# Optimization experiments

Hardware: AMD Instinct MI355X
Metric: run time of the kernel (lower is better)

The kernel has to match this reference:

```python
import jax, jax.numpy as jnp
import numpy as np

D_MODEL = 768
N_HEAD = 12
HEAD_DIM = D_MODEL // N_HEAD
SCALE = HEAD_DIM ** -0.5
B, T = 8, 1024
NEG_INF = -1e9


def setup_inputs() -> dict:
    key = jax.random.key(0)
    ks = jax.random.split(key, 4)
    x = jax.random.normal(ks[0], (B, T, D_MODEL), dtype=jnp.float32)
    W_attn = jax.random.normal(ks[1], (D_MODEL, 3 * D_MODEL), dtype=jnp.float32) * 0.02
    b_attn = jnp.zeros((3 * D_MODEL,), dtype=jnp.float32)
    W_proj = jax.random.normal(ks[2], (D_MODEL, D_MODEL), dtype=jnp.float32) * 0.02
    b_proj = jnp.zeros((D_MODEL,), dtype=jnp.float32)
    return {"x": x, "W_attn": W_attn, "b_attn": b_attn, "W_proj": W_proj, "b_proj": b_proj}


def reference(x, W_attn, b_attn, W_proj, b_proj):
    Bn, Tn, C = x.shape
    # fused QKV projection: [B,T,3C]
    qkv = jnp.einsum('btc,cd->btd', x, W_attn) + b_attn
    q, k, v = jnp.split(qkv, 3, axis=-1)
    # [B, H, T, hd]
    def heads(t):
        return t.reshape(Bn, Tn, N_HEAD, HEAD_DIM).transpose(0, 2, 1, 3)
    q, k, v = heads(q), heads(k), heads(v)
    # scaled dot-product scores [B,H,T,T]
    att = jnp.einsum('bhqd,bhkd->bhqk', q, k) * SCALE
    # causal mask: mask[i,j]=1 where j>i (upper triangle, excluded)
    causal = jnp.tril(jnp.ones((Tn, Tn), dtype=bool))
    att = jnp.where(causal[None, None, :, :], att, NEG_INF)
    att = jax.nn.softmax(att, axis=-1)
    # weighted value sum -> merge heads
    y = jnp.einsum('bhqk,bhkd->bhqd', att, v)
    y = y.transpose(0, 2, 1, 3).reshape(Bn, Tn, C)
    # output projection
    return jnp.einsum('btc,cd->btd', y, W_proj) + b_proj
```

## Files before the change

### kernel.cpp

```cpp
#include <hip/hip_runtime.h>
#include <hip/hip_bf16.h>

#define T_SEQ 1024
#define NBATCH 8
#define NHEAD 12
#define HD 64
#define CDIM 768
#define C3 2304

typedef __attribute__((ext_vector_type(8))) __bf16 bf16x8;
typedef __attribute__((ext_vector_type(4))) __bf16 bf16x4;
typedef __attribute__((ext_vector_type(2))) __bf16 bf16x2;
typedef __attribute__((ext_vector_type(4))) float  f32x4;
typedef __attribute__((ext_vector_type(16))) float f32x16;

__device__ __forceinline__ f32x4 mfma_bf16(bf16x8 a, bf16x8 b, f32x4 c) {
    return __builtin_amdgcn_mfma_f32_16x16x32_bf16(a, b, c, 0, 0, 0);
}
__device__ __forceinline__ f32x16 mfma32(bf16x8 a, bf16x8 b, f32x16 c) {
    return __builtin_amdgcn_mfma_f32_32x32x16_bf16(a, b, c, 0, 0, 0);
}

__device__ __forceinline__ void gload16(const void* g, void* l) {
    __builtin_amdgcn_global_load_lds(
        (const __attribute__((address_space(1))) unsigned int*)g,
        (__attribute__((address_space(3))) unsigned int*)l, 16, 0, 0);
}

#define WAIT_VM(N)  asm volatile("s_waitcnt vmcnt(" #N ")" ::: "memory")
#define WAIT_LGKM0  asm volatile("s_waitcnt lgkmcnt(0)" ::: "memory")

__global__ __launch_bounds__(256) void cvt_f32_bf16(const float* __restrict__ in,
                                                    __bf16* __restrict__ out, int n4) {
    int i = blockIdx.x * 256 + threadIdx.x;
    if (i < n4) {
        float4 v = ((const float4*)in)[i];
        bf16x4 o = { (__bf16)v.x, (__bf16)v.y, (__bf16)v.z, (__bf16)v.w };
        ((bf16x4*)out)[i] = o;
    }
}

__global__ __launch_bounds__(256) void transpose_cvt2(const float* __restrict__ Wa,
                                                      __bf16* __restrict__ Wat,
                                                      const float* __restrict__ Wp,
                                                      __bf16* __restrict__ Wpt) {
    __shared__ float tile[32][33];
    const int bx = blockIdx.x;
    const float* W;  __bf16* Wt;  int C, c0;
    if (bx < 72) { W = Wa; Wt = Wat; C = 2304; c0 = bx * 32; }
    else         { W = Wp; Wt = Wpt; C = 768;  c0 = (bx - 72) * 32; }
    const int r0 = blockIdx.y * 32;
    const int tc = threadIdx.x & 31, tr = threadIdx.x >> 5;
#pragma unroll
    for (int i = 0; i < 4; ++i)
        tile[tr + i * 8][tc] = W[(size_t)(r0 + tr + i * 8) * C + c0 + tc];
    __syncthreads();
#pragma unroll
    for (int i = 0; i < 4; ++i)
        Wt[(size_t)(c0 + tr + i * 8) * 768 + r0 + tc] = (__bf16)tile[tc][tr + i * 8];
}

template<int OUT_BF16>
__global__ __launch_bounds__(256) void gemm_bt(const __bf16* __restrict__ A,
                                               const __bf16* __restrict__ Bt,
                                               const float* __restrict__ bias,
                                               void* __restrict__ Cout,
                                               int M, int N, int K, int nbx) {
    __shared__ __align__(16) __bf16 sA[3][128 * 32];
    __shared__ __align__(16) __bf16 sB[3][128 * 32];
    const int t = threadIdx.x, l = t & 63, w = t >> 6;
    const int l31 = l & 31, lh = l >> 5;
    const int wr = w >> 1, wc = w & 1;
    const int xcd = blockIdx.x & 7;
    const int local = blockIdx.x >> 3;
    const int m0 = (xcd * 8 + (local & 7)) * 128;
    const int n0 = (local >> 3) * 128;

    const int r_st = t >> 2;
    const int sw_st = (r_st & 3) ^ ((r_st >> 2) & 3);
    const int g_off = ((t & 3) ^ sw_st) << 3;
    const int sw_rd = (l31 & 3) ^ ((l31 >> 2) & 3);

    f32x16 acc[2][2];
#pragma unroll
    for (int m = 0; m < 2; ++m)
#pragma unroll
        for (int n = 0; n < 2; ++n)
#pragma unroll
            for (int r = 0; r < 16; ++r) acc[m][n][r] = 0.f;

    const int nk = K >> 5;

#pragma unroll
    for (int s = 0; s < 3; ++s) {
        const int k0 = s << 5;
#pragma unroll
        for (int i = 0; i < 2; ++i) {
            int r = i * 64 + r_st;
            gload16(A + (size_t)(m0 + r) * K + k0 + g_off,
                    (char*)&sA[s][0] + (i * 256 + w * 64) * 16);
            gload16(Bt + (size_t)(n0 + r) * K + k0 + g_off,
                    (char*)&sB[s][0] + (i * 256 + w * 64) * 16);
        }
    }

    int cur = 0;
    for (int kt = 0; kt < nk; ++kt) {
        if (kt + 2 < nk)      WAIT_VM(8);
        else if (kt + 1 < nk) WAIT_VM(4);
        else                  WAIT_VM(0);
        __builtin_amdgcn_s_barrier();

        bf16x8 af[2][2], bg[2][2];
#pragma unroll
        for (int m = 0; m < 2; ++m)
#pragma unroll
            for (int ks = 0; ks < 2; ++ks)
                af[m][ks] = *(const bf16x8*)(&sA[cur][(wr * 64 + m * 32 + l31) * 32
                                                      + ((((ks << 1) | lh) ^ sw_rd) << 3)]);
#pragma unroll
        for (int n = 0; n < 2; ++n)
#pragma unroll
            for (int ks = 0; ks < 2; ++ks)
                bg[n][ks] = *(const bf16x8*)(&sB[cur][(wc * 64 + n * 32 + l31) * 32
                                                      + ((((ks << 1) | lh) ^ sw_rd) << 3)]);

#pragma unroll
        for (int ks = 0; ks < 2; ++ks)
#pragma unroll
            for (int m = 0; m < 2; ++m)
#pragma unroll
                for (int n = 0; n < 2; ++n)
                    acc[m][n] = mfma32(af[m][ks], bg[n][ks], acc[m][n]);

        WAIT_LGKM0;
        __builtin_amdgcn_s_barrier();

        if (kt + 3 < nk) {
            const int k0 = (kt + 3) << 5;
#pragma unroll
            for (int i = 0; i < 2; ++i) {
                int r = i * 64 + r_st;
                gload16(A + (size_t)(m0 + r) * K + k0 + g_off,
                        (char*)&sA[cur][0] + (i * 256 + w * 64) * 16);
                gload16(Bt + (size_t)(n0 + r) * K + k0 + g_off,
                        (char*)&sB[cur][0] + (i * 256 + w * 64) * 16);
            }
        }
        cur = (cur == 2) ? 0 : cur + 1;
    }

#pragma unroll
    for (int n = 0; n < 2; ++n) {
        int col = n0 + wc * 64 + n * 32 + l31;
        float bv = bias[col];
#pragma unroll
        for (int m = 0; m < 2; ++m) {
            int rbase = m0 + wr * 64 + m * 32 + 4 * lh;
#pragma unroll
            for (int r = 0; r < 16; ++r) {
                int row = rbase + (r & 3) + 8 * (r >> 2);
                float v = acc[m][n][r] + bv;
                if (OUT_BF16)
                    ((__bf16*)Cout)[(size_t)row * N + col] = (__bf16)v;
                else
                    ((float*)Cout)[(size_t)row * N + col] = v;
            }
        }
    }
}

__global__ __launch_bounds__(256, 2) void attn_fwd(const __bf16* __restrict__ qkv,
                                                   __bf16* __restrict__ y) {
    const int tid = threadIdx.x, l = tid & 63, w = tid >> 6;
    const int lr = l & 15, lk = l >> 4;
    const int r7 = lr & 7;
    const int bid = blockIdx.x;
    const int pr = bid / 96;
    const int hb = bid % 96;
    const int h = hb % NHEAD;
    const int b = hb / NHEAD;

    __shared__ __align__(16) __bf16 sK[2][64][64];
    __shared__ __align__(16) __bf16 sV[2][64][64];
    __shared__ __align__(16) __bf16 sP[4][16][72];

    const size_t baseQ = (size_t)b * T_SEQ * C3 + h * HD;
    const __bf16* Kp = qkv + baseQ + CDIM;
    const __bf16* Vp = qkv + baseQ + 2 * CDIM;

    const int vk0 = tid >> 3;
    const int vc = (tid & 7) << 3;
    const int vg = tid & 7;
    const int krow = tid >> 3;
    const int kchunk = (tid & 7) ^ ((tid >> 3) & 7);

#pragma unroll 1
    for (int job = 0; job < 2; ++job) {
        const int qt = (job == 0) ? pr : 15 - pr;
        const int q0 = qt * 64;
        const int nt = qt + 1;
        const int q_abs = q0 + w * 16 + lr;

        const size_t rowQ = baseQ + (size_t)(q0 + w * 16 + lr) * C3;
        bf16x8 qa0 = *(const bf16x8*)(qkv + rowQ + lk * 8);
        bf16x8 qa1 = *(const bf16x8*)(qkv + rowQ + 32 + lk * 8);
#pragma unroll
        for (int e = 0; e < 8; ++e) {
            qa0[e] = (__bf16)((float)qa0[e] * 0.125f);
            qa1[e] = (__bf16)((float)qa1[e] * 0.125f);
        }

        f32x4 acc[4];
#pragma unroll
        for (int fd = 0; fd < 4; ++fd) acc[fd] = f32x4{0.f, 0.f, 0.f, 0.f};
        float mrun = -1e30f, lrun = 0.f;

        bf16x8 vreg[2];
#pragma unroll
        for (int i = 0; i < 2; ++i)
            vreg[i] = *(const bf16x8*)(Vp + (size_t)(i * 32 + vk0) * C3 + vc);
#pragma unroll
        for (int i = 0; i < 2; ++i)
            gload16(Kp + (size_t)(i * 32 + krow) * C3 + kchunk * 8,
                    (char*)&sK[0][0][0] + (i * 256 + w * 64) * 16);
#pragma unroll
        for (int i = 0; i < 2; ++i) {
            int key = i * 32 + vk0;
#pragma unroll
            for (int e = 0; e < 8; ++e)
                sV[0][vc + e][key ^ ((e ^ vg) << 3)] = vreg[i][e];
        }
        __syncthreads();

#pragma unroll 1
        for (int t = 0; t < nt; ++t) {
            const int kv0 = t * 64;
            const int cur = t & 1, nxt = cur ^ 1;
            const bool pre = (t + 1 < nt);
            if (pre) {
                const int kvp = kv0 + 64;
#pragma unroll
                for (int i = 0; i < 2; ++i)
                    vreg[i] = *(const bf16x8*)(Vp + (size_t)(kvp + i * 32 + vk0) * C3 + vc);
#pragma unroll
                for (int i = 0; i < 2; ++i)
                    gload16(Kp + (size_t)(kvp + i * 32 + krow) * C3 + kchunk * 8,
                            (char*)&sK[nxt][0][0] + (i * 256 + w * 64) * 16);
            }
            f32x4 s[4];
            __builtin_amdgcn_s_setprio(1);
#pragma unroll
            for (int fc = 0; fc < 4; ++fc) {
                const __bf16* kr = &sK[cur][fc * 16 + lr][0];
                bf16x8 k0 = *(const bf16x8*)(kr + ((lk ^ r7) << 3));
                bf16x8 k1 = *(const bf16x8*)(kr + (((4 + lk) ^ r7) << 3));
                f32x4 z = f32x4{0.f, 0.f, 0.f, 0.f};
                z = mfma_bf16(k0, qa0, z);
                z = mfma_bf16(k1, qa1, z);
                s[fc] = z;
            }
            __builtin_amdgcn_s_setprio(0);
            float ps[4][4];
#pragma unroll
            for (int fc = 0; fc < 4; ++fc)
#pragma unroll
                for (int j = 0; j < 4; ++j) ps[fc][j] = s[fc][j];
            if (t == nt - 1) {
#pragma unroll
                for (int fc = 0; fc < 4; ++fc)
#pragma unroll
                    for (int j = 0; j < 4; ++j) {
                        int key = kv0 + fc * 16 + lk * 4 + j;
                        if (key > q_abs) ps[fc][j] = -1e30f;
                    }
            }
            float mfc[4];
#pragma unroll
            for (int fc = 0; fc < 4; ++fc)
                mfc[fc] = fmaxf(fmaxf(ps[fc][0], ps[fc][1]), fmaxf(ps[fc][2], ps[fc][3]));
            float mt = fmaxf(fmaxf(mfc[0], mfc[1]), fmaxf(mfc[2], mfc[3]));
            mt = fmaxf(mt, __shfl_xor(mt, 16, 64));
            mt = fmaxf(mt, __shfl_xor(mt, 32, 64));
            if (!__all(mt - mrun <= 8.f)) {
                const float mn = fmaxf(mrun, mt);
                const float corr = __expf(mrun - mn);
                mrun = mn;
                lrun *= corr;
                float cj[4];
#pragma unroll
                for (int j = 0; j < 4; ++j) cj[j] = __shfl(corr, lk * 4 + j, 64);
#pragma unroll
                for (int fd = 0; fd < 4; ++fd)
#pragma unroll
                    for (int j = 0; j < 4; ++j) acc[fd][j] *= cj[j];
            }
            float rs = 0.f;
#pragma unroll
            for (int fc = 0; fc < 4; ++fc)
#pragma unroll
                for (int j = 0; j < 4; ++j) {
                    float p = __expf(ps[fc][j] - mrun);
                    ps[fc][j] = p;
                    rs += p;
                }
            rs += __shfl_xor(rs, 16, 64);
            rs += __shfl_xor(rs, 32, 64);
            lrun += rs;
#pragma unroll
            for (int fc = 0; fc < 4; ++fc)
#pragma unroll
                for (int jp = 0; jp < 2; ++jp) {
                    bf16x2 pk = { (__bf16)ps[fc][jp * 2], (__bf16)ps[fc][jp * 2 + 1] };
                    *(bf16x2*)&sP[w][lr][fc * 16 + lk * 4 + jp * 2] = pk;
                }
            __builtin_amdgcn_s_setprio(1);
#pragma unroll
            for (int ks = 0; ks < 2; ++ks) {
                bf16x8 pa = *(const bf16x8*)&sP[w][lr][ks * 32 + lk * 8];
#pragma unroll
                for (int fd = 0; fd < 4; ++fd) {
                    int d = fd * 16 + lr;
                    int sw = ((d & 7) ^ ((d >> 3) & 7)) << 3;
                    bf16x8 vb = *(const bf16x8*)&sV[cur][d][(ks * 32 + lk * 8) ^ sw];
                    acc[fd] = mfma_bf16(pa, vb, acc[fd]);
                }
            }
            __builtin_amdgcn_s_setprio(0);
            if (pre) {
#pragma unroll
                for (int i = 0; i < 2; ++i) {
                    int key = i * 32 + vk0;
#pragma unroll
                    for (int e = 0; e < 8; ++e)
                        sV[nxt][vc + e][key ^ ((e ^ vg) << 3)] = vreg[i][e];
                }
            }
            __syncthreads();
        }

        float linv[4];
#pragma unroll
        for (int j = 0; j < 4; ++j) linv[j] = 1.f / __shfl(lrun, lk * 4 + j, 64);
        const size_t yrow0 = (size_t)(b * T_SEQ + q0 + w * 16 + lk * 4);
#pragma unroll
        for (int fd = 0; fd < 4; ++fd) {
            int col = h * HD + fd * 16 + lr;
#pragma unroll
            for (int j = 0; j < 4; ++j)
                y[(yrow0 + j) * CDIM + col] = (__bf16)(acc[fd][j] * linv[j]);
        }
    }
}

extern "C" void kernel_launch(void* const* d_in, const int* in_sizes, int n_in,
                              void* d_out, int out_size, void* d_ws, size_t ws_size,
                              hipStream_t stream) {
    const float* x      = (const float*)d_in[0];
    const float* W_attn = (const float*)d_in[1];
    const float* b_attn = (const float*)d_in[2];
    const float* W_proj = (const float*)d_in[3];
    const float* b_proj = (const float*)d_in[4];

    __bf16* xb  = (__bf16*)d_ws;
    __bf16* Wat = xb  + (size_t)8192 * 768;
    __bf16* Wpt = Wat + (size_t)2304 * 768;
    __bf16* qkv = Wpt + (size_t)768 * 768;
    __bf16* yb  = qkv + (size_t)8192 * 2304;

    cvt_f32_bf16<<<6144, 256, 0, stream>>>(x, xb, (8192 * 768) / 4);
    transpose_cvt2<<<dim3(96, 24), 256, 0, stream>>>(W_attn, Wat, W_proj, Wpt);

    gemm_bt<1><<<18 * 64, 256, 0, stream>>>(xb, Wat, b_attn, (void*)qkv, 8192, 2304, 768, 18);
    attn_fwd<<<NBATCH * NHEAD * 8, 256, 0, stream>>>(qkv, yb);
    gemm_bt<0><<<6 * 64, 256, 0, stream>>>(yb, Wpt, b_proj, d_out, 8192, 768, 768, 6);
}
```

Baseline: 111.7 us.

## Load QKV GEMM A operand directly to registers, staging only B in LDS

Adds a QKV projection GEMM variant that reads A-operand fragments from global memory straight into registers, double-buffered one k-step ahead, while only the weight tile is staged through LDS with a triple-buffered async pipeline. The aim is to cut LDS traffic and LDS footprint for A and free LDS bandwidth for B reads. In exchange, A reads become uncoalesced-ish per-lane 16B global loads with latency that must be hidden by the one-step prefetch, and the bias-add epilogue uses strided scalar bf16 stores.

```diff
diff --git a/kernel.cpp b/kernel.cpp
--- a/kernel.cpp
+++ b/kernel.cpp
@@ -58,6 +58,111 @@
 #pragma unroll
     for (int i = 0; i < 4; ++i)
         Wt[(size_t)(c0 + tr + i * 8) * 768 + r0 + tc] = (__bf16)tile[tc][tr + i * 8];
+}
+
+#define QKV_STEP(T, AFC, AFN)                                                    \
+    do {                                                                         \
+        const int t_ = (T);                                                      \
+        if (t_ == 0)           WAIT_VM(4);                                       \
+        else if (t_ + 2 < nk)  WAIT_VM(2);                                       \
+        else                   WAIT_VM(0);                                       \
+        __builtin_amdgcn_s_barrier();                                            \
+        if (t_ + 1 < nk) {                                                       \
+            AFN[0][0] = *(const bf16x8*)(pA0 + (t_ + 1) * 32);                   \
+            AFN[0][1] = *(const bf16x8*)(pA0 + (t_ + 1) * 32 + 16);              \
+            AFN[1][0] = *(const bf16x8*)(pA1 + (t_ + 1) * 32);                   \
+            AFN[1][1] = *(const bf16x8*)(pA1 + (t_ + 1) * 32 + 16);              \
+        }                                                                        \
+        bf16x8 bg00 = *(const bf16x8*)(&sB[curb][(wc * 64 + l31) * 32 + ((lh ^ sw_rd) << 3)]);          \
+        bf16x8 bg01 = *(const bf16x8*)(&sB[curb][(wc * 64 + l31) * 32 + (((2 | lh) ^ sw_rd) << 3)]);    \
+        bf16x8 bg10 = *(const bf16x8*)(&sB[curb][(wc * 64 + 32 + l31) * 32 + ((lh ^ sw_rd) << 3)]);     \
+        bf16x8 bg11 = *(const bf16x8*)(&sB[curb][(wc * 64 + 32 + l31) * 32 + (((2 | lh) ^ sw_rd) << 3)]); \
+        acc[0][0] = mfma32(AFC[0][0], bg00, acc[0][0]);                          \
+        acc[0][1] = mfma32(AFC[0][0], bg10, acc[0][1]);                          \
+        acc[1][0] = mfma32(AFC[1][0], bg00, acc[1][0]);                          \
+        acc[1][1] = mfma32(AFC[1][0], bg10, acc[1][1]);                          \
+        acc[0][0] = mfma32(AFC[0][1], bg01, acc[0][0]);                          \
+        acc[0][1] = mfma32(AFC[0][1], bg11, acc[0][1]);                          \
+        acc[1][0] = mfma32(AFC[1][1], bg01, acc[1][0]);                          \
+        acc[1][1] = mfma32(AFC[1][1], bg11, acc[1][1]);                          \
+        WAIT_LGKM0;                                                              \
+        __builtin_amdgcn_s_barrier();                                            \
+        if (t_ + 3 < nk) {                                                       \
+            const int k0 = (t_ + 3) << 5;                                        \
+            gload16(Bt + (size_t)(n0 + r_st) * K + k0 + g_off,                   \
+                    (char*)&sB[curb][0] + (w * 64) * 16);                        \
+            gload16(Bt + (size_t)(n0 + 64 + r_st) * K + k0 + g_off,              \
+                    (char*)&sB[curb][0] + (256 + w * 64) * 16);                  \
+        }                                                                        \
+        curb = (curb == 2) ? 0 : curb + 1;                                       \
+    } while (0)
+
+__global__ __launch_bounds__(256) void gemm_qkv_a2(const __bf16* __restrict__ A,
+                                                   const __bf16* __restrict__ Bt,
+                                                   const float* __restrict__ bias,
+                                                   __bf16* __restrict__ Cout,
+                                                   int M, int N, int K) {
+    __shared__ __align__(16) __bf16 sB[3][128 * 32];
+    const int t = threadIdx.x, l = t & 63, w = t >> 6;
+    const int l31 = l & 31, lh = l >> 5;
+    const int wr = w >> 1, wc = w & 1;
+    const int xcd = blockIdx.x & 7;
+    const int local = blockIdx.x >> 3;
+    const int m0 = (xcd * 8 + (local & 7)) * 128;
+    const int n0 = (local >> 3) * 128;
+
+    const int r_st = t >> 2;
+    const int sw_st = (r_st & 3) ^ ((r_st >> 2) & 3);
+    const int g_off = ((t & 3) ^ sw_st) << 3;
+    const int sw_rd = (l31 & 3) ^ ((l31 >> 2) & 3);
+
+    const __bf16* pA0 = A + (size_t)(m0 + wr * 64 + l31) * K + lh * 8;
+    const __bf16* pA1 = pA0 + (size_t)32 * K;
+
+    f32x16 acc[2][2];
+#pragma unroll
+    for (int m = 0; m < 2; ++m)
+#pragma unroll
+        for (int n = 0; n < 2; ++n)
+#pragma unroll
+            for (int r = 0; r < 16; ++r) acc[m][n][r] = 0.f;
+
+    const int nk = K >> 5;
+    bf16x8 afA[2][2], afB[2][2];
+
+    afA[0][0] = *(const bf16x8*)(pA0);
+    afA[0][1] = *(const bf16x8*)(pA0 + 16);
+    afA[1][0] = *(const bf16x8*)(pA1);
+    afA[1][1] = *(const bf16x8*)(pA1 + 16);
+#pragma unroll
+    for (int s = 0; s < 3; ++s) {
+        const int k0 = s << 5;
+        gload16(Bt + (size_t)(n0 + r_st) * K + k0 + g_off,
+                (char*)&sB[s][0] + (w * 64) * 16);
+        gload16(Bt + (size_t)(n0 + 64 + r_st) * K + k0 + g_off,
+                (char*)&sB[s][0] + (256 + w * 64) * 16);
+    }
+
+    int curb = 0;
+    for (int kt = 0; kt < nk; kt += 2) {
+        QKV_STEP(kt, afA, afB);
+        QKV_STEP(kt + 1, afB, afA);
+    }
+
+#pragma unroll
+    for (int n = 0; n < 2; ++n) {
+        int col = n0 + wc * 64 + n * 32 + l31;
+        float bv = bias[col];
+#pragma unroll
+        for (int m = 0; m < 2; ++m) {
+            int rbase = m0 + wr * 64 + m * 32 + 4 * lh;
+#pragma unroll
+            for (int r = 0; r < 16; ++r) {
+                int row = rbase + (r & 3) + 8 * (r >> 2);
+                Cout[(size_t)row * N + col] = (__bf16)(acc[m][n][r] + bv);
+            }
+        }
+    }
 }
 
 template<int OUT_BF16>
@@ -371,7 +476,7 @@
     cvt_f32_bf16<<<6144, 256, 0, stream>>>(x, xb, (8192 * 768) / 4);
     transpose_cvt2<<<dim3(96, 24), 256, 0, stream>>>(W_attn, Wat, W_proj, Wpt);
 
-    gemm_bt<1><<<18 * 64, 256, 0, stream>>>(xb, Wat, b_attn, (void*)qkv, 8192, 2304, 768, 18);
+    gemm_qkv_a2<<<18 * 64, 256, 0, stream>>>(xb, Wat, b_attn, qkv, 8192, 2304, 768);
     attn_fwd<<<NBATCH * NHEAD * 8, 256, 0, stream>>>(qkv, yb);
     gemm_bt<0><<<6 * 64, 256, 0, stream>>>(yb, Wpt, b_proj, d_out, 8192, 768, 768, 6);
 }
```

Measured after the change: 139.1 us. +24.5%, slower.

## Add quadrant-staged QKV GEMM kernel with interleaved loads and MFMA

Applied to the files above, without the earlier changes.

Replaces the QKV projection GEMM with a new kernel that uses BK=64 double-buffered LDS tiles split into 64-row halves and XOR-swizzled. The next tile's global-to-LDS loads are issued quadrant by quadrant between MFMA groups, which is meant to overlap memory traffic with compute. It also uses 16x16x32 MFMAs and launch bounds targeting two blocks per CU. The cost is more barriers per k-step and a more intricate wait-count schedule that has to stay correct.

```diff
diff --git a/kernel.cpp b/kernel.cpp
--- a/kernel.cpp
+++ b/kernel.cpp
@@ -58,6 +58,124 @@
 #pragma unroll
     for (int i = 0; i < 4; ++i)
         Wt[(size_t)(c0 + tr + i * 8) * 768 + r0 + tc] = (__bf16)tile[tc][tr + i * 8];
+}
+
+__global__ __launch_bounds__(256, 2) void gemm_qkv4(const __bf16* __restrict__ A,
+                                                    const __bf16* __restrict__ Bt,
+                                                    const float* __restrict__ bias,
+                                                    __bf16* __restrict__ Cout,
+                                                    int M, int N, int K) {
+    __shared__ __align__(16) __bf16 sA[2][2][64 * 64];
+    __shared__ __align__(16) __bf16 sB[2][2][64 * 64];
+    const int t = threadIdx.x, l = t & 63, w = t >> 6;
+    const int lr = l & 15, lk = l >> 4;
+    const int r7 = lr & 7;
+    const int wr = w >> 1, wc = w & 1;
+    const int xcd = blockIdx.x & 7;
+    const int local = blockIdx.x >> 3;
+    const int m0 = (xcd * 8 + (local & 7)) * 128;
+    const int n0 = (local >> 3) * 128;
+
+    const int srow = t >> 3;
+    const int g_off = (((t & 7) ^ (srow & 7)) << 3);
+
+#define STG_A(slot, half, kt)                                                      \
+    { _Pragma("unroll") for (int i_ = 0; i_ < 2; ++i_)                             \
+        gload16(A + (size_t)(m0 + (half) * 64 + i_ * 32 + srow) * K + ((kt) << 6) + g_off, \
+                (char*)&sA[slot][half][0] + (i_ * 256 + w * 64) * 16); }
+#define STG_B(slot, half, kt)                                                      \
+    { _Pragma("unroll") for (int i_ = 0; i_ < 2; ++i_)                             \
+        gload16(Bt + (size_t)(n0 + (half) * 64 + i_ * 32 + srow) * K + ((kt) << 6) + g_off, \
+                (char*)&sB[slot][half][0] + (i_ * 256 + w * 64) * 16); }
+#define RD_A(slot, mf, ks) (*(const bf16x8*)&sA[slot][(mf) >> 1]                   \
+        [(wr * 32 + ((mf) & 1) * 16 + lr) * 64 + (((((ks) << 2) | lk) ^ r7) << 3)])
+#define RD_B(slot, nf, ks) (*(const bf16x8*)&sB[slot][(nf) >> 1]                   \
+        [(wc * 32 + ((nf) & 1) * 16 + lr) * 64 + (((((ks) << 2) | lk) ^ r7) << 3)])
+
+    f32x4 acc[4][4];
+#pragma unroll
+    for (int m = 0; m < 4; ++m)
+#pragma unroll
+        for (int n = 0; n < 4; ++n) acc[m][n] = f32x4{0.f, 0.f, 0.f, 0.f};
+
+    const int nk = K >> 6;
+
+    STG_A(0, 0, 0); STG_B(0, 0, 0); STG_B(0, 1, 0); STG_A(0, 1, 0);
+
+    bf16x8 af[4][2], bg[4][2];
+#pragma unroll 1
+    for (int kt = 0; kt < nk; ++kt) {
+        const int sl = kt & 1, ns = sl ^ 1;
+        const bool st = (kt + 1 < nk);
+        WAIT_VM(4);
+        __builtin_amdgcn_s_barrier();
+#pragma unroll
+        for (int ks = 0; ks < 2; ++ks) {
+            af[0][ks] = RD_A(sl, 0, ks);  af[1][ks] = RD_A(sl, 1, ks);
+            bg[0][ks] = RD_B(sl, 0, ks);  bg[1][ks] = RD_B(sl, 1, ks);
+        }
+        if (st) STG_A(ns, 0, kt + 1);
+#pragma unroll
+        for (int ks = 0; ks < 2; ++ks)
+#pragma unroll
+            for (int mf = 0; mf < 2; ++mf)
+#pragma unroll
+                for (int nf = 0; nf < 2; ++nf)
+                    acc[mf][nf] = mfma_bf16(af[mf][ks], bg[nf][ks], acc[mf][nf]);
+        if (st) { WAIT_VM(4); } else { WAIT_VM(2); }
+        __builtin_amdgcn_s_barrier();
+#pragma unroll
+        for (int ks = 0; ks < 2; ++ks) {
+            bg[2][ks] = RD_B(sl, 2, ks);  bg[3][ks] = RD_B(sl, 3, ks);
+        }
+        if (st) STG_B(ns, 0, kt + 1);
+#pragma unroll
+        for (int ks = 0; ks < 2; ++ks)
+#pragma unroll
+            for (int mf = 0; mf < 2; ++mf)
+#pragma unroll
+                for (int nf = 2; nf < 4; ++nf)
+                    acc[mf][nf] = mfma_bf16(af[mf][ks], bg[nf][ks], acc[mf][nf]);
+        if (st) { WAIT_VM(4); } else { WAIT_VM(0); }
+        __builtin_amdgcn_s_barrier();
+#pragma unroll
+        for (int ks = 0; ks < 2; ++ks) {
+            af[2][ks] = RD_A(sl, 2, ks);  af[3][ks] = RD_A(sl, 3, ks);
+        }
+        if (st) STG_B(ns, 1, kt + 1);
+#pragma unroll
+        for (int ks = 0; ks < 2; ++ks)
+#pragma unroll
+            for (int mf = 2; mf < 4; ++mf)
+#pragma unroll
+                for (int nf = 0; nf < 2; ++nf)
+                    acc[mf][nf] = mfma_bf16(af[mf][ks], bg[nf][ks], acc[mf][nf]);
+        if (st) STG_A(ns, 1, kt + 1);
+#pragma unroll
+        for (int ks = 0; ks < 2; ++ks)
+#pragma unroll
+            for (int mf = 2; mf < 4; ++mf)
+#pragma unroll
+                for (int nf = 2; nf < 4; ++nf)
+                    acc[mf][nf] = mfma_bf16(af[mf][ks], bg[nf][ks], acc[mf][nf]);
+    }
+
+#pragma unroll
+    for (int nf = 0; nf < 4; ++nf) {
+        int col = n0 + (nf >> 1) * 64 + wc * 32 + (nf & 1) * 16 + lr;
+        float bv = bias[col];
+#pragma unroll
+        for (int mf = 0; mf < 4; ++mf) {
+            int row0 = m0 + (mf >> 1) * 64 + wr * 32 + (mf & 1) * 16 + lk * 4;
+#pragma unroll
+            for (int j = 0; j < 4; ++j)
+                Cout[(size_t)(row0 + j) * N + col] = (__bf16)(acc[mf][nf][j] + bv);
+        }
+    }
+#undef STG_A
+#undef STG_B
+#undef RD_A
+#undef RD_B
 }
 
 template<int OUT_BF16>
@@ -371,7 +489,7 @@
     cvt_f32_bf16<<<6144, 256, 0, stream>>>(x, xb, (8192 * 768) / 4);
     transpose_cvt2<<<dim3(96, 24), 256, 0, stream>>>(W_attn, Wat, W_proj, Wpt);
 
-    gemm_bt<1><<<18 * 64, 256, 0, stream>>>(xb, Wat, b_attn, (void*)qkv, 8192, 2304, 768, 18);
+    gemm_qkv4<<<18 * 64, 256, 0, stream>>>(xb, Wat, b_attn, qkv, 8192, 2304, 768);
     attn_fwd<<<NBATCH * NHEAD * 8, 256, 0, stream>>>(qkv, yb);
     gemm_bt<0><<<6 * 64, 256, 0, stream>>>(yb, Wpt, b_proj, d_out, 8192, 768, 768, 6);
 }
```

Result: slower. 115.3 us (+3.2%).

## Merge prep kernels into one launch and shrink GEMM M-tile to 64

Applied to the files above, without the earlier changes.

Combines the x conversion and the weight transpose/convert into a single prep launch, saving one kernel launch. Both GEMMs now use 64x128 tiles instead of 128x128, with an adjusted XCD-aware block mapping and matching vmcnt wait counts. The output-projection GEMM goes from 384 to 768 blocks and the QKV GEMM from 1152 to 2304, which should fill the GPU's compute units better. The cost is less data reuse per tile and more global and LDS traffic per FLOP.

```diff
diff --git a/kernel.cpp b/kernel.cpp
--- a/kernel.cpp
+++ b/kernel.cpp
@@ -30,26 +30,27 @@
 #define WAIT_VM(N)  asm volatile("s_waitcnt vmcnt(" #N ")" ::: "memory")
 #define WAIT_LGKM0  asm volatile("s_waitcnt lgkmcnt(0)" ::: "memory")
 
-__global__ __launch_bounds__(256) void cvt_f32_bf16(const float* __restrict__ in,
-                                                    __bf16* __restrict__ out, int n4) {
-    int i = blockIdx.x * 256 + threadIdx.x;
-    if (i < n4) {
-        float4 v = ((const float4*)in)[i];
-        bf16x4 o = { (__bf16)v.x, (__bf16)v.y, (__bf16)v.z, (__bf16)v.w };
-        ((bf16x4*)out)[i] = o;
-    }
-}
-
-__global__ __launch_bounds__(256) void transpose_cvt2(const float* __restrict__ Wa,
-                                                      __bf16* __restrict__ Wat,
-                                                      const float* __restrict__ Wp,
-                                                      __bf16* __restrict__ Wpt) {
+__global__ __launch_bounds__(256) void prep(const float* __restrict__ x,
+                                            __bf16* __restrict__ xb,
+                                            const float* __restrict__ Wa,
+                                            __bf16* __restrict__ Wat,
+                                            const float* __restrict__ Wp,
+                                            __bf16* __restrict__ Wpt) {
     __shared__ float tile[32][33];
     const int bx = blockIdx.x;
+    if (bx < 6144) {
+        int i = bx * 256 + threadIdx.x;
+        float4 v = ((const float4*)x)[i];
+        bf16x4 o = { (__bf16)v.x, (__bf16)v.y, (__bf16)v.z, (__bf16)v.w };
+        ((bf16x4*)xb)[i] = o;
+        return;
+    }
+    const int b2 = bx - 6144;
+    const int gx = b2 % 96, gy = b2 / 96;
     const float* W;  __bf16* Wt;  int C, c0;
-    if (bx < 72) { W = Wa; Wt = Wat; C = 2304; c0 = bx * 32; }
-    else         { W = Wp; Wt = Wpt; C = 768;  c0 = (bx - 72) * 32; }
-    const int r0 = blockIdx.y * 32;
+    if (gx < 72) { W = Wa; Wt = Wat; C = 2304; c0 = gx * 32; }
+    else         { W = Wp; Wt = Wpt; C = 768;  c0 = (gx - 72) * 32; }
+    const int r0 = gy * 32;
     const int tc = threadIdx.x & 31, tr = threadIdx.x >> 5;
 #pragma unroll
     for (int i = 0; i < 4; ++i)
@@ -61,63 +62,57 @@
 }
 
 template<int OUT_BF16>
-__global__ __launch_bounds__(256) void gemm_bt(const __bf16* __restrict__ A,
+__global__ __launch_bounds__(256) void gemm_64(const __bf16* __restrict__ A,
                                                const __bf16* __restrict__ Bt,
                                                const float* __restrict__ bias,
                                                void* __restrict__ Cout,
-                                               int M, int N, int K, int nbx) {
-    __shared__ __align__(16) __bf16 sA[3][128 * 32];
+                                               int M, int N, int K) {
+    __shared__ __align__(16) __bf16 sA[3][64 * 32];
     __shared__ __align__(16) __bf16 sB[3][128 * 32];
     const int t = threadIdx.x, l = t & 63, w = t >> 6;
     const int l31 = l & 31, lh = l >> 5;
     const int wr = w >> 1, wc = w & 1;
     const int xcd = blockIdx.x & 7;
     const int local = blockIdx.x >> 3;
-    const int m0 = (xcd * 8 + (local & 7)) * 128;
-    const int n0 = (local >> 3) * 128;
+    const int m0 = (xcd * 16 + (local & 15)) * 64;
+    const int n0 = (local >> 4) * 128;
 
     const int r_st = t >> 2;
     const int sw_st = (r_st & 3) ^ ((r_st >> 2) & 3);
     const int g_off = ((t & 3) ^ sw_st) << 3;
     const int sw_rd = (l31 & 3) ^ ((l31 >> 2) & 3);
 
-    f32x16 acc[2][2];
-#pragma unroll
-    for (int m = 0; m < 2; ++m)
-#pragma unroll
-        for (int n = 0; n < 2; ++n)
-#pragma unroll
-            for (int r = 0; r < 16; ++r) acc[m][n][r] = 0.f;
+    f32x16 acc[2];
+#pragma unroll
+    for (int n = 0; n < 2; ++n)
+#pragma unroll
+        for (int r = 0; r < 16; ++r) acc[n][r] = 0.f;
 
     const int nk = K >> 5;
 
 #pragma unroll
     for (int s = 0; s < 3; ++s) {
         const int k0 = s << 5;
-#pragma unroll
-        for (int i = 0; i < 2; ++i) {
-            int r = i * 64 + r_st;
-            gload16(A + (size_t)(m0 + r) * K + k0 + g_off,
-                    (char*)&sA[s][0] + (i * 256 + w * 64) * 16);
-            gload16(Bt + (size_t)(n0 + r) * K + k0 + g_off,
+        gload16(A + (size_t)(m0 + r_st) * K + k0 + g_off,
+                (char*)&sA[s][0] + (w * 64) * 16);
+#pragma unroll
+        for (int i = 0; i < 2; ++i)
+            gload16(Bt + (size_t)(n0 + i * 64 + r_st) * K + k0 + g_off,
                     (char*)&sB[s][0] + (i * 256 + w * 64) * 16);
-        }
     }
 
     int cur = 0;
     for (int kt = 0; kt < nk; ++kt) {
-        if (kt + 2 < nk)      WAIT_VM(8);
-        else if (kt + 1 < nk) WAIT_VM(4);
+        if (kt + 2 < nk)      WAIT_VM(6);
+        else if (kt + 1 < nk) WAIT_VM(3);
         else                  WAIT_VM(0);
         __builtin_amdgcn_s_barrier();
 
-        bf16x8 af[2][2], bg[2][2];
-#pragma unroll
-        for (int m = 0; m < 2; ++m)
-#pragma unroll
-            for (int ks = 0; ks < 2; ++ks)
-                af[m][ks] = *(const bf16x8*)(&sA[cur][(wr * 64 + m * 32 + l31) * 32
-                                                      + ((((ks << 1) | lh) ^ sw_rd) << 3)]);
+        bf16x8 af[2], bg[2][2];
+#pragma unroll
+        for (int ks = 0; ks < 2; ++ks)
+            af[ks] = *(const bf16x8*)(&sA[cur][(wr * 32 + l31) * 32
+                                              + ((((ks << 1) | lh) ^ sw_rd) << 3)]);
 #pragma unroll
         for (int n = 0; n < 2; ++n)
 #pragma unroll
@@ -128,24 +123,20 @@
 #pragma unroll
         for (int ks = 0; ks < 2; ++ks)
 #pragma unroll
-            for (int m = 0; m < 2; ++m)
-#pragma unroll
-                for (int n = 0; n < 2; ++n)
-                    acc[m][n] = mfma32(af[m][ks], bg[n][ks], acc[m][n]);
+            for (int n = 0; n < 2; ++n)
+                acc[n] = mfma32(af[ks], bg[n][ks], acc[n]);
 
         WAIT_LGKM0;
         __builtin_amdgcn_s_barrier();
 
         if (kt + 3 < nk) {
             const int k0 = (kt + 3) << 5;
-#pragma unroll
-            for (int i = 0; i < 2; ++i) {
-                int r = i * 64 + r_st;
-                gload16(A + (size_t)(m0 + r) * K + k0 + g_off,
-                        (char*)&sA[cur][0] + (i * 256 + w * 64) * 16);
-                gload16(Bt + (size_t)(n0 + r) * K + k0 + g_off,
+            gload16(A + (size_t)(m0 + r_st) * K + k0 + g_off,
+                    (char*)&sA[cur][0] + (w * 64) * 16);
+#pragma unroll
+            for (int i = 0; i < 2; ++i)
+                gload16(Bt + (size_t)(n0 + i * 64 + r_st) * K + k0 + g_off,
                         (char*)&sB[cur][0] + (i * 256 + w * 64) * 16);
-            }
         }
         cur = (cur == 2) ? 0 : cur + 1;
     }
@@ -154,18 +145,15 @@
     for (int n = 0; n < 2; ++n) {
         int col = n0 + wc * 64 + n * 32 + l31;
         float bv = bias[col];
-#pragma unroll
-        for (int m = 0; m < 2; ++m) {
-            int rbase = m0 + wr * 64 + m * 32 + 4 * lh;
-#pragma unroll
-            for (int r = 0; r < 16; ++r) {
-                int row = rbase + (r & 3) + 8 * (r >> 2);
-                float v = acc[m][n][r] + bv;
-                if (OUT_BF16)
-                    ((__bf16*)Cout)[(size_t)row * N + col] = (__bf16)v;
-                else
-                    ((float*)Cout)[(size_t)row * N + col] = v;
-            }
+        int rbase = m0 + wr * 32 + 4 * lh;
+#pragma unroll
+        for (int r = 0; r < 16; ++r) {
+            int row = rbase + (r & 3) + 8 * (r >> 2);
+            float v = acc[n][r] + bv;
+            if (OUT_BF16)
+                ((__bf16*)Cout)[(size_t)row * N + col] = (__bf16)v;
+            else
+                ((float*)Cout)[(size_t)row * N + col] = v;
         }
     }
 }
@@ -368,10 +356,8 @@
     __bf16* qkv = Wpt + (size_t)768 * 768;
     __bf16* yb  = qkv + (size_t)8192 * 2304;
 
-    cvt_f32_bf16<<<6144, 256, 0, stream>>>(x, xb, (8192 * 768) / 4);
-    transpose_cvt2<<<dim3(96, 24), 256, 0, stream>>>(W_attn, Wat, W_proj, Wpt);
-
-    gemm_bt<1><<<18 * 64, 256, 0, stream>>>(xb, Wat, b_attn, (void*)qkv, 8192, 2304, 768, 18);
+    prep<<<6144 + 2304, 256, 0, stream>>>(x, xb, W_attn, Wat, W_proj, Wpt);
+    gemm_64<1><<<2304, 256, 0, stream>>>(xb, Wat, b_attn, (void*)qkv, 8192, 2304, 768);
     attn_fwd<<<NBATCH * NHEAD * 8, 256, 0, stream>>>(qkv, yb);
-    gemm_bt<0><<<6 * 64, 256, 0, stream>>>(yb, Wpt, b_proj, d_out, 8192, 768, 768, 6);
-}
+    gemm_64<0><<<768, 256, 0, stream>>>(yb, Wpt, b_proj, d_out, 8192, 768, 768);
+}
```

Result: slower. 123.8 us (+10.9%).
